# Kernel tuning notes

Measured on AMD Instinct MI355X. Metric: run time of the kernel, lower is better.

Reference implementation:

```python
import jax, jax.numpy as jnp
import numpy as np

IMG_H, IMG_W = 512.0, 512.0
PRE_NMS = 2000   # training-mode pre_nms_top_n
POST_NMS = 2000  # training-mode post_nms_top_n
NMS_THRESH = 0.7
SCORE_THRESH = 0.0
MIN_SIZE = 0.001


def setup_inputs() -> dict:
    key = jax.random.key(0)
    k1, k2, k3 = jax.random.split(key, 3)
    N = 8
    num_anchors_per_level = (49152, 12288, 3072, 768, 192)  # strides 4..64, 3 anchors/loc on 512^2
    A = sum(num_anchors_per_level)
    cxy = jax.random.uniform(k1, (N, A, 2), minval=0.0, maxval=512.0)
    wh = jax.random.uniform(k2, (N, A, 2), minval=2.0, maxval=120.0)
    proposals = jnp.concatenate([cxy - wh / 2, cxy + wh / 2], axis=-1)  # xyxy
    objectness = jax.random.normal(k3, (N, A), dtype=jnp.float32)
    return {"proposals": proposals, "objectness": objectness,
            "num_anchors_per_level": num_anchors_per_level}


def _box_iou(a, b):
    # a: [K,4], b: [K,4] -> [K,K] pairwise IoU (torchvision box_iou semantics)
    area_a = (a[:, 2] - a[:, 0]) * (a[:, 3] - a[:, 1])
    area_b = (b[:, 2] - b[:, 0]) * (b[:, 3] - b[:, 1])
    lt = jnp.maximum(a[:, None, :2], b[None, :, :2])
    rb = jnp.minimum(a[:, None, 2:], b[None, :, 2:])
    wh = jnp.clip(rb - lt, 0.0)
    inter = wh[..., 0] * wh[..., 1]
    return inter / (area_a[:, None] + area_b[None, :] - inter)


def _per_image(boxes, scores, lvl):
    # boxes [K,4] xyxy, scores [K] (sigmoid probs), lvl [K] int32 level ids
    # 1) clip to image
    x = jnp.clip(boxes[:, 0::2], 0.0, IMG_W)
    y = jnp.clip(boxes[:, 1::2], 0.0, IMG_H)
    boxes = jnp.stack([x[:, 0], y[:, 0], x[:, 1], y[:, 1]], axis=-1)
    # 2) small-box + 3) score-threshold masks (masking instead of boolean indexing)
    ws = boxes[:, 2] - boxes[:, 0]
    hs = boxes[:, 3] - boxes[:, 1]
    valid = (ws >= MIN_SIZE) & (hs >= MIN_SIZE) & (scores >= SCORE_THRESH)
    # 4) batched NMS: offset boxes per level so levels never overlap
    off = lvl.astype(boxes.dtype) * (jnp.max(boxes) + 1.0)
    off_boxes = boxes + off[:, None]
    sm = jnp.where(valid, scores, -jnp.inf)
    order = jnp.argsort(-sm)                 # descending score, invalid last
    boxes_s = boxes[order]
    scores_s = scores[order]
    valid_s = valid[order]
    ob_s = jax.lax.stop_gradient(off_boxes[order])
    K = ob_s.shape[0]
    iou = _box_iou(ob_s, ob_s)               # [K,K], keep decision is non-differentiable
    j = jnp.arange(K)
    def body(i, keep):
        suppress = keep[i] & (iou[i] > NMS_THRESH) & (j > i)
        return keep & ~suppress
    keep = jax.lax.fori_loop(0, K, body, valid_s)
    # 5) top post_nms kept boxes, padded to fixed size with zeros
    rank = jnp.cumsum(keep.astype(jnp.int32)) - 1
    sel_key = jnp.where(keep & (rank < POST_NMS), rank, K)
    idx = jnp.argsort(sel_key)[:POST_NMS]
    out_valid = sel_key[idx] < K
    out_boxes = jnp.where(out_valid[:, None], boxes_s[idx], 0.0)
    out_scores = jnp.where(out_valid, scores_s[idx], 0.0)
    return out_boxes, out_scores


def _forward(proposals, objectness, num_anchors_per_level):
    N = proposals.shape[0]
    napl = [int(n) for n in num_anchors_per_level]
    # per-level, per-image top-k on objectness (get_top_n_idx)
    idx_list, lv_list, off = [], [], 0
    for i, n in enumerate(napl):
        k = min(PRE_NMS, n)
        _, ti = jax.lax.top_k(objectness[:, off:off + n], k)
        idx_list.append(ti + off)
        lv_list.append(jnp.full((k,), i, dtype=jnp.int32))
        off += n
    top_idx = jnp.concatenate(idx_list, axis=1)   # [N, K_total]
    lvls = jnp.concatenate(lv_list)               # [K_total], same for every image
    bidx = jnp.arange(N)[:, None]
    obj = objectness[bidx, top_idx]
    props = proposals[bidx, top_idx]
    scores = jax.nn.sigmoid(obj)
    return jax.vmap(lambda b, s: _per_image(b, s, lvls))(props, scores)


def reference(proposals, objectness, num_anchors_per_level):
    # returns (boxes [N, POST_NMS, 4], scores [N, POST_NMS]); invalid slots zero-padded
    return _forward(proposals, objectness, num_anchors_per_level)
```

## Files before the change

kernel.cpp:

```cpp
#include <hip/hip_runtime.h>
#include <math.h>

#define NIMG 8
#define ATOT 65472
#define KTOT 6960
#define POST 2000
#define TILES_PER_IMG 1668
#define NTILES (NIMG*TILES_PER_IMG)
#define ESEG 1024
#define M_TIE 0.7000000178813934326171875
#define PAD(i) ((i) + ((i) >> 5))

__constant__ int c_NAPL[5]  = {49152,12288,3072,768,192};
__constant__ int c_LOFF[5]  = {0,49152,61440,64512,65280};
__constant__ int c_KSEL[5]  = {2000,2000,2000,768,192};
__constant__ int c_CBASE[5] = {0,2000,4000,6000,6768};
__constant__ int c_GLVL[5]  = {32,32,32,12,3};
__constant__ int c_TILEPFX[6] = {0,528,1056,1584,1662,1668};

__device__ __forceinline__ unsigned f2u(float f){
  unsigned b = __float_as_uint(f);
  return (b & 0x80000000u) ? ~b : (b | 0x80000000u);
}
__device__ __forceinline__ unsigned long long mkkey(unsigned u, unsigned gidx){
  return ((unsigned long long)u << 32) | (unsigned long long)(0xFFFFFFFFu - gidx);
}

extern "C" __global__ void __launch_bounds__(1024)
k_select(const float* __restrict__ prop, const float* __restrict__ obj,
         unsigned long long* __restrict__ cand, float4* __restrict__ cbox,
         unsigned* __restrict__ zzone){
  __shared__ unsigned long long sb[2112];
  __shared__ unsigned hist[4096];
  __shared__ unsigned csum[256];
  __shared__ unsigned h8[256];
  __shared__ unsigned s_b12, s_cumAbove, s_t20, s_cnt;
  int task = blockIdx.x, img = task/5, lvl = task%5;
  int n = c_NAPL[lvl], k = c_KSEL[lvl], tid = threadIdx.x;
  if (task == 0)
    for (int i = tid; i < 1280; i += 1024) zzone[i] = 0u;

  const float4* o4 = (const float4*)(obj + (size_t)img*ATOT + c_LOFF[lvl]);
  int n4 = n >> 2;
  unsigned T = 0u;
  if (k < n){
    for (int i = tid; i < 4096; i += 1024) hist[i] = 0u;
    if (tid < 256) h8[tid] = 0u;
    __syncthreads();
    for (int i = tid; i < n4; i += 1024){
      float4 v = o4[i];
      atomicAdd(&hist[f2u(v.x) >> 20], 1u);
      atomicAdd(&hist[f2u(v.y) >> 20], 1u);
      atomicAdd(&hist[f2u(v.z) >> 20], 1u);
      atomicAdd(&hist[f2u(v.w) >> 20], 1u);
    }
    __syncthreads();
    if (tid < 256){
      unsigned s = 0;
      for (int j = 0; j < 16; ++j) s += hist[tid*16 + j];
      csum[tid] = s;
    }
    __syncthreads();
    if (tid == 0){
      unsigned kk = (unsigned)k, cum = 0, b12 = 0;
      for (int c = 255; c >= 0; --c){
        if (cum + csum[c] >= kk){
          for (int j = 15; j >= 0; --j){
            unsigned bv = hist[c*16 + j];
            if (cum + bv >= kk){ b12 = (unsigned)(c*16 + j); break; }
            cum += bv;
          }
          break;
        }
        cum += csum[c];
      }
      s_b12 = b12; s_cumAbove = cum;
    }
    __syncthreads();
    unsigned b12 = s_b12;
    for (int i = tid; i < n4; i += 1024){
      float4 v = o4[i];
      unsigned ux = f2u(v.x), uy = f2u(v.y), uz = f2u(v.z), uw = f2u(v.w);
      if ((ux >> 20) == b12) atomicAdd(&h8[(ux >> 12) & 255u], 1u);
      if ((uy >> 20) == b12) atomicAdd(&h8[(uy >> 12) & 255u], 1u);
      if ((uz >> 20) == b12) atomicAdd(&h8[(uz >> 12) & 255u], 1u);
      if ((uw >> 20) == b12) atomicAdd(&h8[(uw >> 12) & 255u], 1u);
    }
    __syncthreads();
    if (tid == 0){
      unsigned kk = (unsigned)k, cum = s_cumAbove, t20 = (s_b12 << 8);
      for (int j = 255; j >= 0; --j){
        cum += h8[j];
        if (cum >= kk){ t20 = (s_b12 << 8) | (unsigned)j; break; }
      }
      s_t20 = t20;
    }
    __syncthreads();
    T = s_t20;
  }
  if (tid == 0) s_cnt = 0u;
  __syncthreads();
  int abase = c_LOFF[lvl];
  for (int i = tid; i < n4; i += 1024){
    float4 v = o4[i];
    float vv[4] = {v.x, v.y, v.z, v.w};
    #pragma unroll
    for (int c2 = 0; c2 < 4; ++c2){
      unsigned u = f2u(vv[c2]);
      if ((u >> 12) >= T){
        unsigned p = atomicAdd(&s_cnt, 1u);
        if (p < 2048u) sb[PAD(p)] = mkkey(u, (unsigned)(abase + i*4 + c2));
      }
    }
  }
  __syncthreads();
  int cnt = (int)min(s_cnt, 2048u);
  int m = 256; while (m < k || m < cnt) m <<= 1;
  for (int i = cnt + tid; i < m; i += 1024) sb[PAD(i)] = 0ull;
  __syncthreads();
  for (int size = 2; size <= m; size <<= 1){
    for (int stride = size >> 1; stride > 0; stride >>= 1){
      for (int t = tid; t < (m >> 1); t += 1024){
        int lo = t & (stride - 1);
        int i  = ((t - lo) << 1) + lo;
        int j  = i + stride;
        bool desc = ((i & size) == 0);
        unsigned long long a = sb[PAD(i)], b = sb[PAD(j)];
        if (desc ? (a < b) : (a > b)){ sb[PAD(i)] = b; sb[PAD(j)] = a; }
      }
      __syncthreads();
    }
  }
  const float4* pr = (const float4*)(prop + (size_t)img*ATOT*4);
  for (int i = tid; i < k; i += 1024){
    unsigned long long key = sb[PAD(i)];
    size_t slot = (size_t)img*KTOT + c_CBASE[lvl] + i;
    cand[slot] = key;
    unsigned gidx = 0xFFFFFFFFu - (unsigned)(key & 0xFFFFFFFFull);
    float4 p = pr[gidx];
    cbox[slot] = make_float4(fminf(fmaxf(p.x,0.f),512.f), fminf(fmaxf(p.y,0.f),512.f),
                             fminf(fmaxf(p.z,0.f),512.f), fminf(fmaxf(p.w,0.f),512.f));
  }
}

extern "C" __global__ void __launch_bounds__(64)
k_mask(const float4* __restrict__ cbox, unsigned* __restrict__ ecnt,
       unsigned* __restrict__ eseg, float4* __restrict__ out4, int out_n4){
  __shared__ float4 colb[64];
  __shared__ float  colA[64];
  int bid = blockIdx.x, lane = threadIdx.x;
  if (bid < 313){
    int i = bid*64 + lane;
    if (i < out_n4) out4[i] = make_float4(0.f,0.f,0.f,0.f);
  }
  int img = bid / TILES_PER_IMG, r = bid % TILES_PER_IMG;
  int lvl = 0;
  while (r >= c_TILEPFX[lvl + 1]) ++lvl;
  int t = r - c_TILEPFX[lvl];
  int G = c_GLVL[lvl], k = c_KSEL[lvl];
  int gi = 0;
  while (t >= G - gi){ t -= G - gi; ++gi; }
  int gj = gi + t;
  int task = img*5 + lvl;
  const float4* cb = cbox + (size_t)img*KTOT + c_CBASE[lvl];

  int jj = gj*64 + lane;
  float4 bb = (jj < k) ? cb[jj] : make_float4(0.f,0.f,0.f,0.f);
  colb[lane] = bb;
  colA[lane] = (bb.z - bb.x) * (bb.w - bb.y);
  __syncthreads();

  int i = gi*64 + lane;
  unsigned long long word = 0ull;
  if (i < k){
    float4 a = cb[i];
    float aarea = (a.z - a.x) * (a.w - a.y);
    for (int j = 0; j < 64; ++j){
      float4 b = colb[j];
      float ix = fminf(a.z, b.z) - fmaxf(a.x, b.x);
      float iy = fminf(a.w, b.w) - fmaxf(a.y, b.y);
      float inter = ix * iy;
      float uni = (aarea + colA[j]) - inter;
      bool hit = (ix > 0.f) & (iy > 0.f) & ((double)inter >= M_TIE * (double)uni);
      word |= hit ? (1ull << j) : 0ull;
    }
    if (gi == gj)
      word &= (lane == 63) ? 0ull : (~0ull << (lane + 1));
  }
  int nb = __popcll(word);
  int pfx = nb;
  for (int d = 1; d < 64; d <<= 1){
    int v = __shfl_up(pfx, d);
    if (lane >= d) pfx += v;
  }
  int total = __shfl(pfx, 63);
  if (total > 0){
    unsigned base = 0;
    if (lane == 0) base = atomicAdd(&ecnt[task*32 + gi], (unsigned)total);
    base = __shfl(base, 0);
    unsigned idx = base + (unsigned)(pfx - nb);
    unsigned* ep = eseg + (size_t)(task*32 + gi)*ESEG;
    while (word){
      int j = __ffsll(word) - 1; word &= word - 1;
      if (idx < ESEG) ep[idx] = ((unsigned)i << 16) | (unsigned)(gj*64 + j);
      ++idx;
    }
  }
}

extern "C" __global__ void __launch_bounds__(64)
k_scan(const unsigned long long* __restrict__ cand, const unsigned* __restrict__ ecnt,
       const unsigned* __restrict__ eseg, unsigned long long* __restrict__ clist,
       unsigned* __restrict__ ccnt){
  __shared__ unsigned ledge[6144];
  __shared__ unsigned soff[33], wpfx[33];
  __shared__ unsigned long long sm[64];
  __shared__ unsigned long long remW[32], keepW[32];
  __shared__ unsigned long long s_hasI;
  int task = blockIdx.x, img = task / 5, lvl = task % 5;
  int k = c_KSEL[lvl], nW = c_GLVL[lvl], tid = threadIdx.x;

  if (tid == 0){
    unsigned s = 0;
    for (int w = 0; w < nW; ++w){ soff[w] = s; s += min(ecnt[task*32 + w], (unsigned)ESEG); }
    soff[nW] = s;
  }
  if (tid < 32) remW[tid] = 0ull;
  __syncthreads();
  for (int w = 0; w < nW; ++w){
    unsigned c = soff[w+1] - soff[w];
    const unsigned* ep = eseg + (size_t)(task*32 + w)*ESEG;
    for (unsigned e = tid; e < c; e += 64){
      unsigned p = soff[w] + e;
      if (p < 6144u) ledge[p] = ep[e];
    }
  }
  __syncthreads();

  for (int w = 0; w < nW; ++w){
    unsigned c = soff[w+1] - soff[w];
    if (c == 0) continue;
    const unsigned* ep = eseg + (size_t)(task*32 + w)*ESEG;
    sm[tid] = 0ull;
    if (tid == 0) s_hasI = 0ull;
    __syncthreads();
    for (unsigned e = tid; e < c; e += 64){
      unsigned p = soff[w] + e;
      unsigned ed = (p < 6144u) ? ledge[p] : ep[e];
      int i = (int)(ed >> 16), j = (int)(ed & 0xFFFFu);
      if ((j >> 6) == w){
        atomicOr(&sm[i & 63], 1ull << (j & 63));
        atomicOr(&s_hasI, 1ull << (i & 63));
      }
    }
    __syncthreads();
    if (tid == 0){
      unsigned long long r = remW[w];
      unsigned long long x = s_hasI & ~r;
      while (x){
        int i = __ffsll(x) - 1;
        r |= sm[i];
        x &= ~(1ull << i);
        x &= ~r;
      }
      remW[w] = r;
    }
    __syncthreads();
    unsigned long long keep_w = ~remW[w];
    for (unsigned e = tid; e < c; e += 64){
      unsigned p = soff[w] + e;
      unsigned ed = (p < 6144u) ? ledge[p] : ep[e];
      int i = (int)(ed >> 16), j = (int)(ed & 0xFFFFu), wj = j >> 6;
      if (wj != w && ((keep_w >> (i & 63)) & 1ull))
        atomicOr(&remW[wj], 1ull << (j & 63));
    }
    __syncthreads();
  }

  if (tid < 32){
    unsigned long long v = 0ull;
    if (tid < nW){
      int rem = k - tid*64;
      v = (rem >= 64) ? ~0ull : ((1ull << rem) - 1ull);
    }
    keepW[tid] = v & ~remW[tid];
  }
  __syncthreads();
  if (tid == 0){
    unsigned s = 0;
    for (int w = 0; w < nW; ++w){ wpfx[w] = s; s += (unsigned)__popcll(keepW[w]); }
    ccnt[task] = s;
  }
  __syncthreads();
  size_t base = (size_t)img*KTOT + c_CBASE[lvl];
  for (int i = tid; i < k; i += 64){
    unsigned long long w = keepW[i >> 6];
    if ((w >> (i & 63)) & 1ull){
      unsigned long long lowmask = (i & 63) ? ((1ull << (i & 63)) - 1ull) : 0ull;
      unsigned rank = wpfx[i >> 6] + (unsigned)__popcll(w & lowmask);
      clist[base + rank] = cand[base + i];
    }
  }
}

__device__ __forceinline__ int cntGreater(const unsigned long long* base, int len,
                                          unsigned long long x){
  int lo = 0, hi = len;
  while (lo < hi){
    int mid = (lo + hi) >> 1;
    if (base[mid] > x) lo = mid + 1; else hi = mid;
  }
  return lo;
}

extern "C" __global__ void __launch_bounds__(1024)
k_merge(const float* __restrict__ prop, const float* __restrict__ obj,
        const unsigned long long* __restrict__ clist, const unsigned* __restrict__ ccnt,
        float* __restrict__ out){
  __shared__ unsigned long long keys[KTOT];
  __shared__ int loff[6], lcnt[5];
  int img = blockIdx.x >> 3, eighth = blockIdx.x & 7, tid = threadIdx.x;
  if (tid == 0){
    int s = 0;
    for (int l = 0; l < 5; ++l){ lcnt[l] = (int)ccnt[img*5 + l]; loff[l] = s; s += lcnt[l]; }
    loff[5] = s;
  }
  __syncthreads();
  for (int l = 0; l < 5; ++l){
    size_t gb = (size_t)img*KTOT + c_CBASE[l];
    int c = lcnt[l], lo = loff[l];
    for (int e = tid; e < c; e += 1024) keys[lo + e] = clist[gb + e];
  }
  __syncthreads();
  const float4* pr = (const float4*)(prop + (size_t)img*ATOT*4);
  const float*  o  = obj + (size_t)img*ATOT;
  float* ob = out + (size_t)img*POST*4;
  float* os = out + (size_t)NIMG*POST*4 + (size_t)img*POST;
  int tot = loff[5];
  for (int tt = tid; ; tt += 1024){
    int t = 8*tt + eighth;
    if (t >= tot) break;
    int lvl = 0;
    while (t >= loff[lvl + 1]) ++lvl;
    unsigned long long x = keys[t];
    int pos = t - loff[lvl];
    for (int l = 0; l < 5; ++l){
      if (l == lvl) continue;
      pos += cntGreater(keys + loff[l], lcnt[l], x);
    }
    if (pos < POST){
      unsigned gidx = 0xFFFFFFFFu - (unsigned)(x & 0xFFFFFFFFull);
      float4 p = pr[gidx];
      ob[pos*4 + 0] = fminf(fmaxf(p.x, 0.f), 512.f);
      ob[pos*4 + 1] = fminf(fmaxf(p.y, 0.f), 512.f);
      ob[pos*4 + 2] = fminf(fmaxf(p.z, 0.f), 512.f);
      ob[pos*4 + 3] = fminf(fmaxf(p.w, 0.f), 512.f);
      double sgm = 1.0 / (1.0 + exp(-(double)o[gidx]));
      os[pos] = (float)sgm;
    }
  }
}

extern "C" void kernel_launch(void* const* d_in, const int* in_sizes, int n_in,
                              void* d_out, int out_size, void* d_ws, size_t ws_size,
                              hipStream_t stream){
  const float* prop = (const float*)d_in[0];
  const float* obj  = (const float*)d_in[1];
  char* ws = (char*)d_ws;
  unsigned*           ecnt = (unsigned*)(ws);
  unsigned*           ccnt = (unsigned*)(ws + 5120);
  unsigned long long* cand = (unsigned long long*)(ws + 5632);
  unsigned long long* clist= (unsigned long long*)(ws + 451072);
  float4*             cbox = (float4*)(ws + 896512);
  unsigned*           eseg = (unsigned*)(ws + 1787392);

  int out_n4 = out_size / 4;
  hipLaunchKernelGGL(k_select, dim3(40),  dim3(1024), 0, stream, prop, obj, cand, cbox, ecnt);
  hipLaunchKernelGGL(k_mask,   dim3(NTILES), dim3(64), 0, stream, cbox, ecnt, eseg,
                     (float4*)d_out, out_n4);
  hipLaunchKernelGGL(k_scan,   dim3(40),  dim3(64),   0, stream, cand, ecnt, eseg, clist, ccnt);
  hipLaunchKernelGGL(k_merge,  dim3(64),  dim3(1024), 0, stream, prop, obj, clist, ccnt, (float*)d_out);
}
```

Before: 200.3 us.

## Fuse scan and merge kernels per image; add float fast-path for IoU threshold

Merges the per-level suppression scan and the cross-level merge into one kernel with one block per image, five waves each scanning one level in shared memory and writing survivors directly to shared keys. This drops a launch and the global clist/ccnt round trip. The merge now runs on only 8 blocks instead of 64, so that phase has less parallelism. The IoU test in the mask kernel uses float bounds around 0.7 and falls back to the double comparison only when a wave has an ambiguous pair.

```diff
diff --git a/kernel.cpp b/kernel.cpp
--- a/kernel.cpp
+++ b/kernel.cpp
@@ -8,8 +8,10 @@
 #define TILES_PER_IMG 1668
 #define NTILES (NIMG*TILES_PER_IMG)
 #define ESEG 1024
+#define LEDGE 2048
 #define M_TIE 0.7000000178813934326171875
 #define PAD(i) ((i) + ((i) >> 5))
+#define WAVE_SYNC() asm volatile("s_waitcnt lgkmcnt(0)" ::: "memory")
 
 __constant__ int c_NAPL[5]  = {49152,12288,3072,768,192};
 __constant__ int c_LOFF[5]  = {0,49152,61440,64512,65280};
@@ -181,7 +183,13 @@
       float iy = fminf(a.w, b.w) - fmaxf(a.y, b.y);
       float inter = ix * iy;
       float uni = (aarea + colA[j]) - inter;
-      bool hit = (ix > 0.f) & (iy > 0.f) & ((double)inter >= M_TIE * (double)uni);
+      bool base = (ix > 0.f) & (iy > 0.f);
+      bool hi  = inter >= 0.701f * uni;
+      bool lo  = inter <  0.699f * uni;
+      bool hit = base & hi;
+      bool amb = base & (!hi) & (!lo);
+      if (__any(amb))
+        hit = hit | (amb & ((double)inter >= M_TIE * (double)uni));
       word |= hit ? (1ull << j) : 0ull;
     }
     if (gi == gj)
@@ -208,101 +216,6 @@
   }
 }
 
-extern "C" __global__ void __launch_bounds__(64)
-k_scan(const unsigned long long* __restrict__ cand, const unsigned* __restrict__ ecnt,
-       const unsigned* __restrict__ eseg, unsigned long long* __restrict__ clist,
-       unsigned* __restrict__ ccnt){
-  __shared__ unsigned ledge[6144];
-  __shared__ unsigned soff[33], wpfx[33];
-  __shared__ unsigned long long sm[64];
-  __shared__ unsigned long long remW[32], keepW[32];
-  __shared__ unsigned long long s_hasI;
-  int task = blockIdx.x, img = task / 5, lvl = task % 5;
-  int k = c_KSEL[lvl], nW = c_GLVL[lvl], tid = threadIdx.x;
-
-  if (tid == 0){
-    unsigned s = 0;
-    for (int w = 0; w < nW; ++w){ soff[w] = s; s += min(ecnt[task*32 + w], (unsigned)ESEG); }
-    soff[nW] = s;
-  }
-  if (tid < 32) remW[tid] = 0ull;
-  __syncthreads();
-  for (int w = 0; w < nW; ++w){
-    unsigned c = soff[w+1] - soff[w];
-    const unsigned* ep = eseg + (size_t)(task*32 + w)*ESEG;
-    for (unsigned e = tid; e < c; e += 64){
-      unsigned p = soff[w] + e;
-      if (p < 6144u) ledge[p] = ep[e];
-    }
-  }
-  __syncthreads();
-
-  for (int w = 0; w < nW; ++w){
-    unsigned c = soff[w+1] - soff[w];
-    if (c == 0) continue;
-    const unsigned* ep = eseg + (size_t)(task*32 + w)*ESEG;
-    sm[tid] = 0ull;
-    if (tid == 0) s_hasI = 0ull;
-    __syncthreads();
-    for (unsigned e = tid; e < c; e += 64){
-      unsigned p = soff[w] + e;
-      unsigned ed = (p < 6144u) ? ledge[p] : ep[e];
-      int i = (int)(ed >> 16), j = (int)(ed & 0xFFFFu);
-      if ((j >> 6) == w){
-        atomicOr(&sm[i & 63], 1ull << (j & 63));
-        atomicOr(&s_hasI, 1ull << (i & 63));
-      }
-    }
-    __syncthreads();
-    if (tid == 0){
-      unsigned long long r = remW[w];
-      unsigned long long x = s_hasI & ~r;
-      while (x){
-        int i = __ffsll(x) - 1;
-        r |= sm[i];
-        x &= ~(1ull << i);
-        x &= ~r;
-      }
-      remW[w] = r;
-    }
-    __syncthreads();
-    unsigned long long keep_w = ~remW[w];
-    for (unsigned e = tid; e < c; e += 64){
-      unsigned p = soff[w] + e;
-      unsigned ed = (p < 6144u) ? ledge[p] : ep[e];
-      int i = (int)(ed >> 16), j = (int)(ed & 0xFFFFu), wj = j >> 6;
-      if (wj != w && ((keep_w >> (i & 63)) & 1ull))
-        atomicOr(&remW[wj], 1ull << (j & 63));
-    }
-    __syncthreads();
-  }
-
-  if (tid < 32){
-    unsigned long long v = 0ull;
-    if (tid < nW){
-      int rem = k - tid*64;
-      v = (rem >= 64) ? ~0ull : ((1ull << rem) - 1ull);
-    }
-    keepW[tid] = v & ~remW[tid];
-  }
-  __syncthreads();
-  if (tid == 0){
-    unsigned s = 0;
-    for (int w = 0; w < nW; ++w){ wpfx[w] = s; s += (unsigned)__popcll(keepW[w]); }
-    ccnt[task] = s;
-  }
-  __syncthreads();
-  size_t base = (size_t)img*KTOT + c_CBASE[lvl];
-  for (int i = tid; i < k; i += 64){
-    unsigned long long w = keepW[i >> 6];
-    if ((w >> (i & 63)) & 1ull){
-      unsigned long long lowmask = (i & 63) ? ((1ull << (i & 63)) - 1ull) : 0ull;
-      unsigned rank = wpfx[i >> 6] + (unsigned)__popcll(w & lowmask);
-      clist[base + rank] = cand[base + i];
-    }
-  }
-}
-
 __device__ __forceinline__ int cntGreater(const unsigned long long* base, int len,
                                           unsigned long long x){
   int lo = 0, hi = len;
@@ -314,22 +227,108 @@
 }
 
 extern "C" __global__ void __launch_bounds__(1024)
-k_merge(const float* __restrict__ prop, const float* __restrict__ obj,
-        const unsigned long long* __restrict__ clist, const unsigned* __restrict__ ccnt,
-        float* __restrict__ out){
+k_finish(const float* __restrict__ prop, const float* __restrict__ obj,
+         const unsigned long long* __restrict__ cand, const unsigned* __restrict__ ecnt,
+         const unsigned* __restrict__ eseg, float* __restrict__ out){
   __shared__ unsigned long long keys[KTOT];
-  __shared__ int loff[6], lcnt[5];
-  int img = blockIdx.x >> 3, eighth = blockIdx.x & 7, tid = threadIdx.x;
+  __shared__ unsigned long long sm[5][64];
+  __shared__ unsigned long long remW[5][32];
+  __shared__ unsigned long long hasI[5];
+  __shared__ unsigned ledge[5][LEDGE];
+  __shared__ unsigned soff[5][33];
+  __shared__ int lcnt[5], loff[6];
+  int img = blockIdx.x, tid = threadIdx.x;
+  int wv = tid >> 6, lane = tid & 63;
+
+  if (wv < 5){
+    int lvl = wv, task = img*5 + lvl;
+    int k = c_KSEL[lvl], nW = c_GLVL[lvl];
+    if (lane == 0){
+      unsigned s = 0;
+      for (int w = 0; w < nW; ++w){ soff[lvl][w] = s; s += min(ecnt[task*32 + w], (unsigned)ESEG); }
+      soff[lvl][nW] = s;
+    }
+    if (lane < 32) remW[lvl][lane] = 0ull;
+    WAVE_SYNC();
+    for (int w = 0; w < nW; ++w){
+      unsigned c = soff[lvl][w+1] - soff[lvl][w];
+      const unsigned* ep = eseg + (size_t)(task*32 + w)*ESEG;
+      for (unsigned e = lane; e < c; e += 64){
+        unsigned p = soff[lvl][w] + e;
+        if (p < (unsigned)LEDGE) ledge[lvl][p] = ep[e];
+      }
+    }
+    WAVE_SYNC();
+    for (int w = 0; w < nW; ++w){
+      unsigned c = soff[lvl][w+1] - soff[lvl][w];
+      if (c == 0) continue;
+      const unsigned* ep = eseg + (size_t)(task*32 + w)*ESEG;
+      sm[lvl][lane] = 0ull;
+      if (lane == 0) hasI[lvl] = 0ull;
+      WAVE_SYNC();
+      for (unsigned e = lane; e < c; e += 64){
+        unsigned p = soff[lvl][w] + e;
+        unsigned ed = (p < (unsigned)LEDGE) ? ledge[lvl][p] : ep[e];
+        int i = (int)(ed >> 16), j = (int)(ed & 0xFFFFu);
+        if ((j >> 6) == w){
+          atomicOr(&sm[lvl][i & 63], 1ull << (j & 63));
+          atomicOr(&hasI[lvl], 1ull << (i & 63));
+        }
+      }
+      WAVE_SYNC();
+      if (lane == 0){
+        unsigned long long rr = remW[lvl][w];
+        unsigned long long x = hasI[lvl] & ~rr;
+        while (x){
+          int i = __ffsll(x) - 1;
+          rr |= sm[lvl][i];
+          x &= ~(1ull << i);
+          x &= ~rr;
+        }
+        remW[lvl][w] = rr;
+      }
+      WAVE_SYNC();
+      unsigned long long keep_w = ~remW[lvl][w];
+      for (unsigned e = lane; e < c; e += 64){
+        unsigned p = soff[lvl][w] + e;
+        unsigned ed = (p < (unsigned)LEDGE) ? ledge[lvl][p] : ep[e];
+        int i = (int)(ed >> 16), j = (int)(ed & 0xFFFFu), wj = j >> 6;
+        if (wj != w && ((keep_w >> (i & 63)) & 1ull))
+          atomicOr(&remW[lvl][wj], 1ull << (j & 63));
+      }
+      WAVE_SYNC();
+    }
+    if (lane < 32){
+      unsigned long long v = 0ull;
+      if (lane < nW){
+        int rem = k - lane*64;
+        v = (rem >= 64) ? ~0ull : ((1ull << rem) - 1ull);
+      }
+      remW[lvl][lane] = v & ~remW[lvl][lane];
+    }
+    WAVE_SYNC();
+    if (lane == 0){
+      unsigned s = 0;
+      for (int w = 0; w < nW; ++w){ soff[lvl][w] = s; s += (unsigned)__popcll(remW[lvl][w]); }
+      lcnt[lvl] = (int)s;
+    }
+    WAVE_SYNC();
+    size_t gbase = (size_t)img*KTOT + c_CBASE[lvl];
+    for (int i = lane; i < k; i += 64){
+      unsigned long long w = remW[lvl][i >> 6];
+      if ((w >> (i & 63)) & 1ull){
+        unsigned long long lowmask = (i & 63) ? ((1ull << (i & 63)) - 1ull) : 0ull;
+        unsigned rank = soff[lvl][i >> 6] + (unsigned)__popcll(w & lowmask);
+        keys[c_CBASE[lvl] + rank] = cand[gbase + i];
+      }
+    }
+  }
+  __syncthreads();
+
   if (tid == 0){
     int s = 0;
-    for (int l = 0; l < 5; ++l){ lcnt[l] = (int)ccnt[img*5 + l]; loff[l] = s; s += lcnt[l]; }
+    for (int l = 0; l < 5; ++l){ loff[l] = s; s += lcnt[l]; }
     loff[5] = s;
-  }
-  __syncthreads();
-  for (int l = 0; l < 5; ++l){
-    size_t gb = (size_t)img*KTOT + c_CBASE[l];
-    int c = lcnt[l], lo = loff[l];
-    for (int e = tid; e < c; e += 1024) keys[lo + e] = clist[gb + e];
   }
   __syncthreads();
   const float4* pr = (const float4*)(prop + (size_t)img*ATOT*4);
@@ -337,16 +336,15 @@
   float* ob = out + (size_t)img*POST*4;
   float* os = out + (size_t)NIMG*POST*4 + (size_t)img*POST;
   int tot = loff[5];
-  for (int tt = tid; ; tt += 1024){
-    int t = 8*tt + eighth;
-    if (t >= tot) break;
+  for (int t = tid; t < tot; t += 1024){
     int lvl = 0;
     while (t >= loff[lvl + 1]) ++lvl;
-    unsigned long long x = keys[t];
-    int pos = t - loff[lvl];
+    int e = t - loff[lvl];
+    unsigned long long x = keys[c_CBASE[lvl] + e];
+    int pos = e;
     for (int l = 0; l < 5; ++l){
       if (l == lvl) continue;
-      pos += cntGreater(keys + loff[l], lcnt[l], x);
+      pos += cntGreater(keys + c_CBASE[l], lcnt[l], x);
     }
     if (pos < POST){
       unsigned gidx = 0xFFFFFFFFu - (unsigned)(x & 0xFFFFFFFFull);
@@ -368,16 +366,14 @@
   const float* obj  = (const float*)d_in[1];
   char* ws = (char*)d_ws;
   unsigned*           ecnt = (unsigned*)(ws);
-  unsigned*           ccnt = (unsigned*)(ws + 5120);
   unsigned long long* cand = (unsigned long long*)(ws + 5632);
-  unsigned long long* clist= (unsigned long long*)(ws + 451072);
-  float4*             cbox = (float4*)(ws + 896512);
-  unsigned*           eseg = (unsigned*)(ws + 1787392);
+  float4*             cbox = (float4*)(ws + 451072);
+  unsigned*           eseg = (unsigned*)(ws + 1341952);
 
   int out_n4 = out_size / 4;
   hipLaunchKernelGGL(k_select, dim3(40),  dim3(1024), 0, stream, prop, obj, cand, cbox, ecnt);
   hipLaunchKernelGGL(k_mask,   dim3(NTILES), dim3(64), 0, stream, cbox, ecnt, eseg,
                      (float4*)d_out, out_n4);
-  hipLaunchKernelGGL(k_scan,   dim3(40),  dim3(64),   0, stream, cand, ecnt, eseg, clist, ccnt);
-  hipLaunchKernelGGL(k_merge,  dim3(64),  dim3(1024), 0, stream, prop, obj, clist, ccnt, (float*)d_out);
-}
+  hipLaunchKernelGGL(k_finish, dim3(NIMG), dim3(1024), 0, stream, prop, obj, cand, ecnt,
+                     eseg, (float*)d_out);
+}
```

New measurement: 225.7 us. 12.6% more time.
